# Kernel optimization log

Measured on AMD Instinct MI355X. Metric: run time of the kernel, lower is better.

Reference implementation:

```python
import jax, jax.numpy as jnp
import numpy as np

# ---- static config (must match init_kwargs) ----
DIM = 256
DIM_K = 16
N = 32          # window size: hh = ww = N
HEADS = 8
DIM_OUT = 256
DIM_U = 1
DIM_V = DIM_OUT // HEADS  # 32
EPS = 1e-5
N2 = N * N


def _calc_rel_pos(n):
    # pos: (n*n, 2) of (i, j) coords, rel: (n*n, n*n, 2) shifted by n-1
    pos = np.stack(np.meshgrid(np.arange(n), np.arange(n), indexing='ij'), axis=-1).reshape(-1, 2)
    rel = pos[None, :, :] - pos[:, None, :] + (n - 1)
    return rel.astype(np.int32)

_REL = _calc_rel_pos(N)  # (N2, N2, 2)


def _cplx(re, im):
    return jax.lax.complex(re, im)


def _complex_bn(x, scale, shift):
    # x: (b, c, m) complex. Complex batchnorm: var = E[x^2] - E[x]^2 (complex square).
    mean = x.mean(axis=(0, 2))                       # (c,)
    var = (x ** 2).mean(axis=(0, 2)) - mean ** 2     # (c,) complex
    xn = (x - mean[None, :, None]) / jnp.sqrt(var + EPS)[None, :, None]
    return scale[None, :, None] * xn + shift[None, :, None]


def setup_inputs() -> dict:
    key = jax.random.key(0)
    ks = jax.random.split(key, 18)
    f = jnp.float32
    b = 16
    mk = lambda k, shape, s=1.0: (jax.random.normal(k, shape, dtype=f) * s)
    inp = {
        'x_re': mk(ks[0], (b, DIM, N, N)),
        'x_im': mk(ks[1], (b, DIM, N, N)),
        # 1x1 conv weights, stored as (out_ch, in_ch)
        'wq_re': mk(ks[2], (DIM_K * HEADS, DIM), DIM ** -0.5),
        'wq_im': mk(ks[3], (DIM_K * HEADS, DIM), DIM ** -0.5),
        'wk_re': mk(ks[4], (DIM_K * DIM_U, DIM), DIM ** -0.5),
        'wk_im': mk(ks[5], (DIM_K * DIM_U, DIM), DIM ** -0.5),
        'wv_re': mk(ks[6], (DIM_V * DIM_U, DIM), DIM ** -0.5),
        'wv_im': mk(ks[7], (DIM_V * DIM_U, DIM), DIM ** -0.5),
        # complex BN affine params (init: scale=1+0j, shift=0)
        'qs_re': jnp.ones((DIM_K * HEADS,), f),
        'qs_im': jnp.zeros((DIM_K * HEADS,), f),
        'qb_re': jnp.zeros((DIM_K * HEADS,), f),
        'qb_im': jnp.zeros((DIM_K * HEADS,), f),
        'vs_re': jnp.ones((DIM_V * DIM_U,), f),
        'vs_im': jnp.zeros((DIM_V * DIM_U,), f),
        'vb_re': jnp.zeros((DIM_V * DIM_U,), f),
        'vb_im': jnp.zeros((DIM_V * DIM_U,), f),
        # rel-pos embedding table (2n-1, 2n-1, k, u)
        'emb_re': mk(ks[8], (2 * N - 1, 2 * N - 1, DIM_K, DIM_U)),
        'emb_im': mk(ks[9], (2 * N - 1, 2 * N - 1, DIM_K, DIM_U)),
    }
    return inp


def reference(x_re, x_im, wq_re, wq_im, wk_re, wk_im, wv_re, wv_im,
              qs_re, qs_im, qb_re, qb_im, vs_re, vs_im, vb_re, vb_im,
              emb_re, emb_im):
    x = _cplx(x_re, x_im)                       # (b, c, N, N)
    b = x.shape[0]
    xf = x.reshape(b, DIM, N2)                  # (b, c, m)

    wq = _cplx(wq_re, wq_im)
    wk = _cplx(wk_re, wk_im)
    wv = _cplx(wv_re, wv_im)

    q = jnp.einsum('oc,bcm->bom', wq, xf)       # (b, k*h, m)
    k = jnp.einsum('oc,bcm->bom', wk, xf)       # (b, k*u, m)
    v = jnp.einsum('oc,bcm->bom', wv, xf)       # (b, v*u, m)

    q = _complex_bn(q, _cplx(qs_re, qs_im), _cplx(qb_re, qb_im))
    v = _complex_bn(v, _cplx(vs_re, vs_im), _cplx(vb_re, vb_im))

    q = q.reshape(b, HEADS, DIM_K, N2)          # b h k n
    k = k.reshape(b, DIM_U, DIM_K, N2)          # b u k m
    v = v.reshape(b, DIM_U, DIM_V, N2)          # b u v m

    k = jax.nn.softmax(jnp.abs(k), axis=-1).astype(jnp.complex64)

    lam_c = jnp.einsum('bukm,buvm->bkv', k, v)          # content lambda
    Yc = jnp.einsum('bhkn,bkv->bhvn', q, lam_c)

    emb = _cplx(emb_re, emb_im)
    remb = emb[_REL[..., 0], _REL[..., 1]]              # (n, m, k, u) gathered
    lam_p = jnp.einsum('nmku,buvm->bnkv', remb, v)      # positional lambdas
    Yp = jnp.einsum('bhkn,bnkv->bhvn', q, lam_p)

    Y = Yc + Yp                                          # (b, h, v, n)
    out = Y.reshape(b, HEADS * DIM_V, N, N)             # b (h v) hh ww
    return out
```

## Files before the change

### kernel.cpp

```cpp
#include <hip/hip_runtime.h>
#include <math.h>

#define DIMC 256
#define NCH  176
#define MM   1024
#define BB   16
#define KD   16
#define HH   8
#define VD   32
#define EPSV 1e-5
#define OPAD 192

typedef short short8 __attribute__((ext_vector_type(8)));
typedef float f32x4  __attribute__((ext_vector_type(4)));
typedef unsigned u32x4v __attribute__((ext_vector_type(4)));

union frag8 { unsigned u[4]; short8 s; u32x4v v; };

__device__ __forceinline__ unsigned bf16rne(float f) {
    unsigned u = __float_as_uint(f);
    unsigned r = u + 0x7FFFu + ((u >> 16) & 1u);
    return r >> 16;
}
__device__ __forceinline__ float bf16tof(unsigned h) {
    return __uint_as_float(h << 16);
}

#define GL2LDS16(g, l) __builtin_amdgcn_global_load_lds( \
    (const __attribute__((address_space(1))) unsigned*)(g), \
    (__attribute__((address_space(3))) unsigned*)(l), 16, 0, 0)
#define GL2LDS4(g, l) __builtin_amdgcn_global_load_lds( \
    (const __attribute__((address_space(1))) unsigned*)(g), \
    (__attribute__((address_space(3))) unsigned*)(l), 4, 0, 0)

__global__ __launch_bounds__(256) void k_wprep(
    const float* __restrict__ wq_re, const float* __restrict__ wq_im,
    const float* __restrict__ wk_re, const float* __restrict__ wk_im,
    const float* __restrict__ wv_re, const float* __restrict__ wv_im,
    unsigned* __restrict__ Wpk)
{
    int idx = blockIdx.x * 256 + threadIdx.x;
    if (idx >= OPAD * 128) return;
    int o = idx >> 7, j = idx & 127;
    int c0 = 2 * j;
    float r0 = 0.f, r1 = 0.f, i0 = 0.f, i1 = 0.f;
    if (o < 128) {
        r0 = wq_re[o * DIMC + c0]; r1 = wq_re[o * DIMC + c0 + 1];
        i0 = wq_im[o * DIMC + c0]; i1 = wq_im[o * DIMC + c0 + 1];
    } else if (o < 144) {
        int oo = o - 128;
        r0 = wk_re[oo * DIMC + c0]; r1 = wk_re[oo * DIMC + c0 + 1];
        i0 = wk_im[oo * DIMC + c0]; i1 = wk_im[oo * DIMC + c0 + 1];
    } else if (o < 176) {
        int oo = o - 144;
        r0 = wv_re[oo * DIMC + c0]; r1 = wv_re[oo * DIMC + c0 + 1];
        i0 = wv_im[oo * DIMC + c0]; i1 = wv_im[oo * DIMC + c0 + 1];
    }
    unsigned rh0 = bf16rne(r0), rh1 = bf16rne(r1);
    unsigned ih0 = bf16rne(i0), ih1 = bf16rne(i1);
    float rl0 = r0 - bf16tof(rh0), rl1 = r1 - bf16tof(rh1);
    float il0 = i0 - bf16tof(ih0), il1 = i1 - bf16tof(ih1);
    Wpk[0 * OPAD * 128 + idx] = rh0 | (rh1 << 16);
    Wpk[1 * OPAD * 128 + idx] = ih0 | (ih1 << 16);
    Wpk[2 * OPAD * 128 + idx] = bf16rne(rl0) | (bf16rne(rl1) << 16);
    Wpk[3 * OPAD * 128 + idx] = bf16rne(il0) | (bf16rne(il1) << 16);
}

__global__ __launch_bounds__(256, 2) void k_proj(
    const float* __restrict__ x_re, const float* __restrict__ x_im,
    const unsigned* __restrict__ Wpk,
    float2* __restrict__ O)
{
    const int m0  = blockIdx.x * 32;
    const int b   = blockIdx.y;
    const int tid = threadIdx.x;
    const int w    = tid >> 6;
    const int lane = tid & 63;
    const int quad = lane >> 4;
    const int col  = lane & 15;
    const int mt = w & 1, og = w >> 1;

    __shared__ __align__(16) unsigned Wsh[4 * OPAD * 16];
    __shared__ __align__(16) unsigned Xsh[4 * 32 * 20];

    f32x4 accR[6], accI[6];
#pragma unroll
    for (int t = 0; t < 6; ++t) {
        accR[t] = (f32x4){0.f, 0.f, 0.f, 0.f};
        accI[t] = (f32x4){0.f, 0.f, 0.f, 0.f};
    }

    const int ms = tid & 31;
    const int cps = tid >> 5;

#pragma unroll 1
    for (int kk = 0; kk < 8; ++kk) {
#pragma unroll
        for (int p = 0; p < 12; ++p) {
            int idx = p * 256 + tid;
            int plane = idx / 768;
            int rem = idx - plane * 768;
            int row = rem >> 2, seg = rem & 3;
            u32x4v d = *(const u32x4v*)&Wpk[(size_t)plane * (OPAD * 128) + row * 128 + kk * 16 + seg * 4];
            *(u32x4v*)&Wsh[(plane * OPAD + row) * 16 + seg * 4] = d;
        }
#pragma unroll
        for (int p = 0; p < 2; ++p) {
            int cp = cps + p * 8;
            int c  = kk * 32 + cp * 2;
            size_t base = ((size_t)(b * DIMC + c)) * MM + m0 + ms;
            float r0 = x_re[base],      i0 = x_im[base];
            float r1 = x_re[base + MM], i1 = x_im[base + MM];
            unsigned rh0 = bf16rne(r0), rh1 = bf16rne(r1);
            unsigned ih0 = bf16rne(i0), ih1 = bf16rne(i1);
            float rl0 = r0 - bf16tof(rh0), rl1 = r1 - bf16tof(rh1);
            float il0 = i0 - bf16tof(ih0), il1 = i1 - bf16tof(ih1);
            Xsh[0 * 640 + ms * 20 + cp] = rh0 | (rh1 << 16);
            Xsh[1 * 640 + ms * 20 + cp] = ih0 | (ih1 << 16);
            Xsh[2 * 640 + ms * 20 + cp] = bf16rne(rl0) | (bf16rne(rl1) << 16);
            Xsh[3 * 640 + ms * 20 + cp] = bf16rne(il0) | (bf16rne(il1) << 16);
        }
        __syncthreads();

        int mrow = mt * 16 + col;
        short8 Xrh = *(const short8*)&Xsh[0 * 640 + mrow * 20 + quad * 4];
        short8 Xih = *(const short8*)&Xsh[1 * 640 + mrow * 20 + quad * 4];
        short8 Xrl = *(const short8*)&Xsh[2 * 640 + mrow * 20 + quad * 4];
        short8 Xil = *(const short8*)&Xsh[3 * 640 + mrow * 20 + quad * 4];

#pragma unroll
        for (int ot = 0; ot < 6; ++ot) {
            int orow = (og * 6 + ot) * 16 + col;
            frag8 Arh, Aih, Arl, Ail, Anh, Anl;
            Arh.s = *(const short8*)&Wsh[(0 * OPAD + orow) * 16 + quad * 4];
            Aih.s = *(const short8*)&Wsh[(1 * OPAD + orow) * 16 + quad * 4];
            Arl.s = *(const short8*)&Wsh[(2 * OPAD + orow) * 16 + quad * 4];
            Ail.s = *(const short8*)&Wsh[(3 * OPAD + orow) * 16 + quad * 4];
#pragma unroll
            for (int i = 0; i < 4; ++i) {
                Anh.u[i] = Aih.u[i] ^ 0x80008000u;
                Anl.u[i] = Ail.u[i] ^ 0x80008000u;
            }
            accR[ot] = __builtin_amdgcn_mfma_f32_16x16x32_bf16(Arh.s, Xrh, accR[ot], 0, 0, 0);
            accR[ot] = __builtin_amdgcn_mfma_f32_16x16x32_bf16(Anh.s, Xih, accR[ot], 0, 0, 0);
            accR[ot] = __builtin_amdgcn_mfma_f32_16x16x32_bf16(Arh.s, Xrl, accR[ot], 0, 0, 0);
            accR[ot] = __builtin_amdgcn_mfma_f32_16x16x32_bf16(Anh.s, Xil, accR[ot], 0, 0, 0);
            accR[ot] = __builtin_amdgcn_mfma_f32_16x16x32_bf16(Arl.s, Xrh, accR[ot], 0, 0, 0);
            accR[ot] = __builtin_amdgcn_mfma_f32_16x16x32_bf16(Anl.s, Xih, accR[ot], 0, 0, 0);
            accI[ot] = __builtin_amdgcn_mfma_f32_16x16x32_bf16(Arh.s, Xih, accI[ot], 0, 0, 0);
            accI[ot] = __builtin_amdgcn_mfma_f32_16x16x32_bf16(Aih.s, Xrh, accI[ot], 0, 0, 0);
            accI[ot] = __builtin_amdgcn_mfma_f32_16x16x32_bf16(Arh.s, Xil, accI[ot], 0, 0, 0);
            accI[ot] = __builtin_amdgcn_mfma_f32_16x16x32_bf16(Aih.s, Xrl, accI[ot], 0, 0, 0);
            accI[ot] = __builtin_amdgcn_mfma_f32_16x16x32_bf16(Arl.s, Xih, accI[ot], 0, 0, 0);
            accI[ot] = __builtin_amdgcn_mfma_f32_16x16x32_bf16(Ail.s, Xrh, accI[ot], 0, 0, 0);
        }
        __syncthreads();
    }

#pragma unroll
    for (int ot = 0; ot < 6; ++ot) {
        int gto = og * 6 + ot;
        if (gto >= 11) continue;
#pragma unroll
        for (int r = 0; r < 4; ++r) {
            int o = gto * 16 + quad * 4 + r;
            O[((size_t)(b * NCH + o)) * MM + m0 + mt * 16 + col] =
                make_float2(accR[ot][r], accI[ot][r]);
        }
    }
}

__global__ __launch_bounds__(256) void k_bnstats(
    const float2* __restrict__ O,
    const float* __restrict__ qs_re, const float* __restrict__ qs_im,
    const float* __restrict__ qb_re, const float* __restrict__ qb_im,
    const float* __restrict__ vs_re, const float* __restrict__ vs_im,
    const float* __restrict__ vb_re, const float* __restrict__ vb_im,
    float4* __restrict__ stats)
{
    const int ch  = blockIdx.x;
    const int o   = (ch < 128) ? ch : (144 + ch - 128);
    const int tid = threadIdx.x;

    double sr = 0, si = 0, sq = 0, sri = 0;
    for (int idx = tid; idx < BB * MM; idx += 256) {
        int b = idx >> 10, m = idx & 1023;
        float2 val = O[((size_t)(b * NCH + o)) * MM + m];
        double r = val.x, ii = val.y;
        sr += r; si += ii; sq += r * r - ii * ii; sri += r * ii;
    }
    __shared__ double red[4][256];
    red[0][tid] = sr; red[1][tid] = si; red[2][tid] = sq; red[3][tid] = sri;
    __syncthreads();
    for (int s = 128; s > 0; s >>= 1) {
        if (tid < s) {
            red[0][tid] += red[0][tid + s]; red[1][tid] += red[1][tid + s];
            red[2][tid] += red[2][tid + s]; red[3][tid] += red[3][tid + s];
        }
        __syncthreads();
    }
    if (tid == 0) {
        const double inv = 1.0 / (double)(BB * MM);
        double mr = red[0][0] * inv, mi = red[1][0] * inv;
        double vr = red[2][0] * inv - (mr * mr - mi * mi) + EPSV;
        double vi = 2.0 * (red[3][0] * inv - mr * mi);
        double rad = sqrt(vr * vr + vi * vi);
        double wr  = sqrt(fmax(0.5 * (rad + vr), 0.0));
        double wi  = sqrt(fmax(0.5 * (rad - vr), 0.0));
        if (vi < 0) wi = -wi;
        double den = wr * wr + wi * wi;
        double ivr = wr / den, ivi = -wi / den;
        double scr, sci, shr, shi;
        if (ch < 128) { scr = qs_re[ch]; sci = qs_im[ch]; shr = qb_re[ch]; shi = qb_im[ch]; }
        else { int i2 = ch - 128; scr = vs_re[i2]; sci = vs_im[i2]; shr = vb_re[i2]; shi = vb_im[i2]; }
        double Ar = scr * ivr - sci * ivi;
        double Ai = scr * ivi + sci * ivr;
        double Br = shr - (Ar * mr - Ai * mi);
        double Bi = shi - (Ar * mi + Ai * mr);
        stats[ch] = make_float4((float)Ar, (float)Ai, (float)Br, (float)Bi);
    }
}

__global__ __launch_bounds__(256) void k_bnapply(
    const float4* __restrict__ stats, float2* __restrict__ O,
    unsigned* __restrict__ VR, unsigned* __restrict__ VI)
{
    int ch = blockIdx.x, b = blockIdx.y;
    int o  = (ch < 128) ? ch : (144 + ch - 128);
    float4 s = stats[ch];
    float2* row = O + ((size_t)(b * NCH + o)) * MM;
    int tid = threadIdx.x;
    for (int mm = tid; mm < 512; mm += 256) {
        float4 two = *(float4*)&row[2 * mm];
        float nr0 = s.x * two.x - s.y * two.y + s.z;
        float ni0 = s.x * two.y + s.y * two.x + s.w;
        float nr1 = s.x * two.z - s.y * two.w + s.z;
        float ni1 = s.x * two.w + s.y * two.z + s.w;
        *(float4*)&row[2 * mm] = make_float4(nr0, ni0, nr1, ni1);
        if (ch >= 128) {
            int bv = b * VD + (ch - 128);
            int cC = mm >> 4, off = mm & 15;
            int u = off >> 2, oo = off & 3;
            int sl = (((u ^ (bv & 3)) << 2) | oo);
            size_t idx = ((size_t)cC * 512 + bv) * 16 + sl;
            VR[idx] = bf16rne(nr0) | (bf16rne(nr1) << 16);
            VI[idx] = bf16rne(ni0) | (bf16rne(ni1) << 16);
        }
    }
}

__global__ __launch_bounds__(256) void k_softlam(
    const float2* __restrict__ O, float2* __restrict__ lamc)
{
    int kc = blockIdx.x, b = blockIdx.y;
    const float2* row = O + ((size_t)(b * NCH + 128 + kc)) * MM;
    int tid = threadIdx.x;
    __shared__ float red[256];
    __shared__ float skl[1024];

    float mag[4]; float mx = -1e30f;
#pragma unroll
    for (int j = 0; j < 4; ++j) {
        float2 v = row[tid + j * 256];
        mag[j] = sqrtf(v.x * v.x + v.y * v.y);
        mx = fmaxf(mx, mag[j]);
    }
    red[tid] = mx; __syncthreads();
    for (int s = 128; s > 0; s >>= 1) { if (tid < s) red[tid] = fmaxf(red[tid], red[tid + s]); __syncthreads(); }
    mx = red[0]; __syncthreads();
    float e[4]; float sum = 0.f;
#pragma unroll
    for (int j = 0; j < 4; ++j) { e[j] = expf(mag[j] - mx); sum += e[j]; }
    red[tid] = sum; __syncthreads();
    for (int s = 128; s > 0; s >>= 1) { if (tid < s) red[tid] += red[tid + s]; __syncthreads(); }
    float inv = 1.f / red[0];
#pragma unroll
    for (int j = 0; j < 4; ++j) skl[tid + j * 256] = e[j] * inv;
    __syncthreads();

    int v = tid >> 3, s8 = tid & 7;
    const float2* vrow = O + ((size_t)(b * NCH + 144 + v)) * MM;
    float ar = 0.f, ai = 0.f;
    for (int i = 0; i < 128; ++i) {
        int m = s8 * 128 + i;
        float wgt = skl[m]; float2 vv = vrow[m];
        ar += wgt * vv.x; ai += wgt * vv.y;
    }
    __shared__ float2 part[32][8];
    part[v][s8] = make_float2(ar, ai);
    __syncthreads();
    if (tid < 32) {
        float2 t = part[tid][0];
#pragma unroll
        for (int j = 1; j < 8; ++j) { t.x += part[tid][j].x; t.y += part[tid][j].y; }
        lamc[((size_t)(b * KD + kc)) * VD + tid] = t;
    }
}

__global__ __launch_bounds__(256) void k_eprepD(
    const float* __restrict__ er, const float* __restrict__ ei,
    unsigned* __restrict__ embD)
{
    int idx = blockIdx.x * 256 + threadIdx.x;
    if (idx >= 8 * 63 * 768) return;
    int s   = idx % 48;
    int k   = (idx / 48) % 16;
    int di  = (idx / 768) % 63;
    int win = idx / (768 * 63);
    int u_s = s >> 2, o = s & 3;
    int p   = (((k >> 1) & 1) << 1) | ((k >> 2) & 1);
    int dj2 = ((u_s ^ p) << 2) | o;
    int dj  = 28 - win * 4 + dj2;
    unsigned val = 0;
    if (dj <= 62) {
        int e = (di * 63 + dj) * 16 + k;
        val = bf16rne(er[e]) | (bf16rne(ei[e]) << 16);
    }
    embD[idx] = val;
}

__global__ __launch_bounds__(256, 2) void k_main(
    const float2* __restrict__ O,
    const unsigned* __restrict__ embD,
    const unsigned* __restrict__ VbfR,
    const unsigned* __restrict__ VbfI,
    const float2* __restrict__ lamc,
    float* __restrict__ out, int cplx)
{
    const int tid  = threadIdx.x;
    const int w    = tid >> 6;
    const int lane = tid & 63;
    const int quad = lane >> 4;
    const int col  = lane & 15;

    const int n0  = blockIdx.x * 4;
    const int bvq = blockIdx.y;
    const int b0  = bvq * 4;
    const int ni  = n0 >> 5;
    const int nj0 = n0 & 31;
    const int win = nj0 >> 2;

    __shared__ __align__(16) unsigned shraw[2 * 4864];
    __shared__ __align__(16) float2 qsh[2048];

#pragma unroll
    for (int it = 0; it < 8; ++it) {
        int idx = it * 256 + tid;
        int g = idx & 3, ch = (idx >> 2) & 127, bl = idx >> 9;
        qsh[idx] = O[((size_t)((b0 + bl) * NCH + ch)) * MM + n0 + g];
    }

    f32x4 accr[4][2], acci[4][2];
#pragma unroll
    for (int g = 0; g < 4; ++g)
#pragma unroll
        for (int t = 0; t < 2; ++t) {
            accr[g][t] = (f32x4){0.f, 0.f, 0.f, 0.f};
            acci[g][t] = (f32x4){0.f, 0.f, 0.f, 0.f};
        }

    const unsigned* vR0 = VbfR + (size_t)bvq * 2048 + w * 512 + lane * 4;
    const unsigned* vI0 = VbfI + (size_t)bvq * 2048 + w * 512 + lane * 4;
    const unsigned* eD0 = embD + (size_t)win * (63 * 768) + w * 64 + lane;

    const int p     = (((col >> 1) & 1) << 1) | ((col >> 2) & 1);
    const int aBase = col * 48;
    const int a0 = aBase + (((2 * quad)     ^ p) << 2);
    const int a1 = aBase + (((2 * quad + 1) ^ p) << 2);
    const int a2 = aBase + (((2 * quad + 2) ^ p) << 2);
    const int bswz  = (quad ^ (col & 3)) << 2;
    const int rowb0 = (w * 32 + col) * 16 + bswz;
    const int rowb1 = (w * 32 + 16 + col) * 16 + bswz;

    {
        unsigned* vr = shraw;
        unsigned* vi = shraw + 2048;
        unsigned* es = shraw + 4096;
        GL2LDS16(vR0,       vr + w * 512);
        GL2LDS16(vR0 + 256, vr + w * 512 + 256);
        GL2LDS16(vI0,       vi + w * 512);
        GL2LDS16(vI0 + 256, vi + w * 512 + 256);
        const unsigned* gE = eD0 + (size_t)(31 - ni) * 768;
        GL2LDS4(gE,       es + w * 64);
        GL2LDS4(gE + 256, es + 256 + w * 64);
        GL2LDS4(gE + 512, es + 512 + w * 64);
    }

#pragma unroll 1
    for (int c = 0; c < 32; ++c) {
        __syncthreads();

        if (c + 1 < 32) {
            unsigned* vr = shraw + ((c + 1) & 1) * 4864;
            unsigned* vi = vr + 2048;
            unsigned* es = vr + 4096;
            const unsigned* gR = vR0 + (size_t)(c + 1) * 8192;
            const unsigned* gI = vI0 + (size_t)(c + 1) * 8192;
            GL2LDS16(gR,       vr + w * 512);
            GL2LDS16(gR + 256, vr + w * 512 + 256);
            GL2LDS16(gI,       vi + w * 512);
            GL2LDS16(gI + 256, vi + w * 512 + 256);
            const unsigned* gE = eD0 + (size_t)(c + 1 - ni + 31) * 768;
            GL2LDS4(gE,       es + w * 64);
            GL2LDS4(gE + 256, es + 256 + w * 64);
            GL2LDS4(gE + 512, es + 512 + w * 64);
        }

        const unsigned* vr = shraw + (c & 1) * 4864;
        const unsigned* vi = vr + 2048;
        const unsigned* es = vr + 4096;

        short8 Br0 = *(const short8*)&vr[rowb0];
        short8 Br1 = *(const short8*)&vr[rowb1];
        short8 Bi0 = *(const short8*)&vi[rowb0];
        short8 Bi1 = *(const short8*)&vi[rowb1];

        u32x4v W0 = *(const u32x4v*)&es[a0];
        u32x4v W1 = *(const u32x4v*)&es[a1];
        u32x4v W2 = *(const u32x4v*)&es[a2];
        unsigned W[12] = { W0.x, W0.y, W0.z, W0.w,
                           W1.x, W1.y, W1.z, W1.w,
                           W2.x, W2.y, W2.z, W2.w };

#pragma unroll
        for (int g = 0; g < 4; ++g) {
            const int o = 3 - g;
            union { unsigned u[4]; short8 s; } Rr, Ri, Rin;
            Rr.u[0] = __builtin_amdgcn_perm(W[o + 1], W[o + 0], 0x05040100u);
            Rr.u[1] = __builtin_amdgcn_perm(W[o + 3], W[o + 2], 0x05040100u);
            Rr.u[2] = __builtin_amdgcn_perm(W[o + 5], W[o + 4], 0x05040100u);
            Rr.u[3] = __builtin_amdgcn_perm(W[o + 7], W[o + 6], 0x05040100u);
            Ri.u[0] = __builtin_amdgcn_perm(W[o + 1], W[o + 0], 0x07060302u);
            Ri.u[1] = __builtin_amdgcn_perm(W[o + 3], W[o + 2], 0x07060302u);
            Ri.u[2] = __builtin_amdgcn_perm(W[o + 5], W[o + 4], 0x07060302u);
            Ri.u[3] = __builtin_amdgcn_perm(W[o + 7], W[o + 6], 0x07060302u);
            Rin.u[0] = Ri.u[0] ^ 0x80008000u;
            Rin.u[1] = Ri.u[1] ^ 0x80008000u;
            Rin.u[2] = Ri.u[2] ^ 0x80008000u;
            Rin.u[3] = Ri.u[3] ^ 0x80008000u;
            accr[g][0] = __builtin_amdgcn_mfma_f32_16x16x32_bf16(Rr.s,  Br0, accr[g][0], 0, 0, 0);
            accr[g][0] = __builtin_amdgcn_mfma_f32_16x16x32_bf16(Rin.s, Bi0, accr[g][0], 0, 0, 0);
            acci[g][0] = __builtin_amdgcn_mfma_f32_16x16x32_bf16(Rr.s,  Bi0, acci[g][0], 0, 0, 0);
            acci[g][0] = __builtin_amdgcn_mfma_f32_16x16x32_bf16(Ri.s,  Br0, acci[g][0], 0, 0, 0);
            accr[g][1] = __builtin_amdgcn_mfma_f32_16x16x32_bf16(Rr.s,  Br1, accr[g][1], 0, 0, 0);
            accr[g][1] = __builtin_amdgcn_mfma_f32_16x16x32_bf16(Rin.s, Bi1, accr[g][1], 0, 0, 0);
            acci[g][1] = __builtin_amdgcn_mfma_f32_16x16x32_bf16(Rr.s,  Bi1, acci[g][1], 0, 0, 0);
            acci[g][1] = __builtin_amdgcn_mfma_f32_16x16x32_bf16(Ri.s,  Br1, acci[g][1], 0, 0, 0);
        }
    }

    float2 lcv[2][4];
#pragma unroll
    for (int t = 0; t < 2; ++t) {
        int bvl = w * 32 + t * 16 + col;
        int bloc = b0 + (bvl >> 5), v = bvl & 31;
#pragma unroll
        for (int r = 0; r < 4; ++r)
            lcv[t][r] = lamc[((size_t)(bloc * KD + quad * 4 + r)) * VD + v];
    }

    float2* lamt = (float2*)shraw;
    const int col128 = tid & 127;
    const int hb = (tid >> 7) * 4;
    const int bl = col128 >> 5, vY = col128 & 31;
    const int bY = b0 + bl;
    float2* op2 = (float2*)out;
#pragma unroll
    for (int g = 0; g < 4; ++g) {
        __syncthreads();
#pragma unroll
        for (int t = 0; t < 2; ++t) {
            int bvl = w * 32 + t * 16 + col;
#pragma unroll
            for (int r = 0; r < 4; ++r) {
                int k = quad * 4 + r;
                lamt[k * 128 + bvl] = make_float2(accr[g][t][r] + lcv[t][r].x,
                                                  acci[g][t][r] + lcv[t][r].y);
            }
        }
        __syncthreads();
        float yr[4], yi[4];
#pragma unroll
        for (int h = 0; h < 4; ++h) { yr[h] = 0.f; yi[h] = 0.f; }
#pragma unroll
        for (int k = 0; k < 16; ++k) {
            float2 l = lamt[k * 128 + col128];
#pragma unroll
            for (int h = 0; h < 4; ++h) {
                float2 q = qsh[(bl * 128 + (hb + h) * 16 + k) * 4 + g];
                yr[h] += q.x * l.x - q.y * l.y;
                yi[h] += q.x * l.y + q.y * l.x;
            }
        }
        int n = n0 + g;
        if (cplx) {
#pragma unroll
            for (int h = 0; h < 4; ++h)
                op2[((size_t)(bY * 256 + (hb + h) * 32 + vY)) * MM + n] = make_float2(yr[h], yi[h]);
        } else {
#pragma unroll
            for (int h = 0; h < 4; ++h)
                out[((size_t)(bY * 256 + (hb + h) * 32 + vY)) * MM + n] = yr[h];
        }
    }
}

extern "C" void kernel_launch(void* const* d_in, const int* in_sizes, int n_in,
                              void* d_out, int out_size, void* d_ws, size_t ws_size,
                              hipStream_t stream)
{
    const float* x_re  = (const float*)d_in[0];
    const float* x_im  = (const float*)d_in[1];
    const float* wq_re = (const float*)d_in[2];
    const float* wq_im = (const float*)d_in[3];
    const float* wk_re = (const float*)d_in[4];
    const float* wk_im = (const float*)d_in[5];
    const float* wv_re = (const float*)d_in[6];
    const float* wv_im = (const float*)d_in[7];
    const float* qs_re = (const float*)d_in[8];
    const float* qs_im = (const float*)d_in[9];
    const float* qb_re = (const float*)d_in[10];
    const float* qb_im = (const float*)d_in[11];
    const float* vs_re = (const float*)d_in[12];
    const float* vs_im = (const float*)d_in[13];
    const float* vb_re = (const float*)d_in[14];
    const float* vb_im = (const float*)d_in[15];
    const float* emb_re = (const float*)d_in[16];
    const float* emb_im = (const float*)d_in[17];

    float* ws = (float*)d_ws;
    const size_t O_OFF  = 0;
    const size_t ST_OFF = O_OFF + (size_t)BB * NCH * MM * 2;
    const size_t LC_OFF = ST_OFF + 640;
    const size_t WP_OFF = LC_OFF + 16384;
    const size_t VR_OFF = WP_OFF + 98304;
    const size_t VI_OFF = VR_OFF + 262144;
    const size_t ED_OFF = VI_OFF + 262144;

    float2*   O     = (float2*)(ws + O_OFF);
    float4*   stats = (float4*)(ws + ST_OFF);
    float2*   lamc  = (float2*)(ws + LC_OFF);
    unsigned* Wpk   = (unsigned*)(ws + WP_OFF);
    unsigned* VbfR  = (unsigned*)(ws + VR_OFF);
    unsigned* VbfI  = (unsigned*)(ws + VI_OFF);
    unsigned* embD  = (unsigned*)(ws + ED_OFF);
    float*    outp  = (float*)d_out;

    int cplx = (out_size >= 2 * BB * 256 * MM) ? 1 : 0;

    k_wprep<<<dim3(96), 256, 0, stream>>>(wq_re, wq_im, wk_re, wk_im,
                                          wv_re, wv_im, Wpk);
    k_eprepD<<<dim3(1512), 256, 0, stream>>>(emb_re, emb_im, embD);
    k_proj<<<dim3(32, BB), 256, 0, stream>>>(x_re, x_im, Wpk, O);
    k_bnstats<<<dim3(160), 256, 0, stream>>>(O, qs_re, qs_im, qb_re, qb_im,
                                             vs_re, vs_im, vb_re, vb_im, stats);
    k_bnapply<<<dim3(160, BB), 256, 0, stream>>>(stats, O, VbfR, VbfI);
    k_softlam<<<dim3(KD, BB), 256, 0, stream>>>(O, lamc);
    k_main<<<dim3(256, 4), 256, 0, stream>>>(O, embD, VbfR, VbfI, lamc, outp, cplx);
}
```

Before: 282.9 us.

## Load V fragments directly to registers, vectorize X loads, shrink LDS footprint

```diff
diff --git a/kernel.cpp b/kernel.cpp
--- a/kernel.cpp
+++ b/kernel.cpp
@@ -29,9 +29,6 @@
 #define GL2LDS16(g, l) __builtin_amdgcn_global_load_lds( \
     (const __attribute__((address_space(1))) unsigned*)(g), \
     (__attribute__((address_space(3))) unsigned*)(l), 16, 0, 0)
-#define GL2LDS4(g, l) __builtin_amdgcn_global_load_lds( \
-    (const __attribute__((address_space(1))) unsigned*)(g), \
-    (__attribute__((address_space(3))) unsigned*)(l), 4, 0, 0)
 
 __global__ __launch_bounds__(256) void k_wprep(
     const float* __restrict__ wq_re, const float* __restrict__ wq_im,
@@ -90,8 +87,9 @@
         accI[t] = (f32x4){0.f, 0.f, 0.f, 0.f};
     }
 
-    const int ms = tid & 31;
-    const int cps = tid >> 5;
+    const int cl = tid >> 3;
+    const int m4 = (tid & 7) * 4;
+    const int cp = cl >> 1, half = cl & 1;
 
 #pragma unroll 1
     for (int kk = 0; kk < 8; ++kk) {
@@ -104,21 +102,24 @@
             u32x4v d = *(const u32x4v*)&Wpk[(size_t)plane * (OPAD * 128) + row * 128 + kk * 16 + seg * 4];
             *(u32x4v*)&Wsh[(plane * OPAD + row) * 16 + seg * 4] = d;
         }
-#pragma unroll
-        for (int p = 0; p < 2; ++p) {
-            int cp = cps + p * 8;
-            int c  = kk * 32 + cp * 2;
-            size_t base = ((size_t)(b * DIMC + c)) * MM + m0 + ms;
-            float r0 = x_re[base],      i0 = x_im[base];
-            float r1 = x_re[base + MM], i1 = x_im[base + MM];
-            unsigned rh0 = bf16rne(r0), rh1 = bf16rne(r1);
-            unsigned ih0 = bf16rne(i0), ih1 = bf16rne(i1);
-            float rl0 = r0 - bf16tof(rh0), rl1 = r1 - bf16tof(rh1);
-            float il0 = i0 - bf16tof(ih0), il1 = i1 - bf16tof(ih1);
-            Xsh[0 * 640 + ms * 20 + cp] = rh0 | (rh1 << 16);
-            Xsh[1 * 640 + ms * 20 + cp] = ih0 | (ih1 << 16);
-            Xsh[2 * 640 + ms * 20 + cp] = bf16rne(rl0) | (bf16rne(rl1) << 16);
-            Xsh[3 * 640 + ms * 20 + cp] = bf16rne(il0) | (bf16rne(il1) << 16);
+        {
+            size_t base = ((size_t)(b * DIMC + kk * 32 + cl)) * MM + m0 + m4;
+            float4 xr = *(const float4*)&x_re[base];
+            float4 xi = *(const float4*)&x_im[base];
+            unsigned short* xs = (unsigned short*)Xsh;
+            const float* xrf = (const float*)&xr;
+            const float* xif = (const float*)&xi;
+#pragma unroll
+            for (int j = 0; j < 4; ++j) {
+                float r = xrf[j], iv = xif[j];
+                unsigned rh = bf16rne(r), ih = bf16rne(iv);
+                float rl = r - bf16tof(rh), il = iv - bf16tof(ih);
+                int m = m4 + j;
+                xs[(0 * 640 + m * 20 + cp) * 2 + half] = (unsigned short)rh;
+                xs[(1 * 640 + m * 20 + cp) * 2 + half] = (unsigned short)ih;
+                xs[(2 * 640 + m * 20 + cp) * 2 + half] = (unsigned short)bf16rne(rl);
+                xs[(3 * 640 + m * 20 + cp) * 2 + half] = (unsigned short)bf16rne(il);
+            }
         }
         __syncthreads();
 
@@ -240,9 +241,7 @@
         if (ch >= 128) {
             int bv = b * VD + (ch - 128);
             int cC = mm >> 4, off = mm & 15;
-            int u = off >> 2, oo = off & 3;
-            int sl = (((u ^ (bv & 3)) << 2) | oo);
-            size_t idx = ((size_t)cC * 512 + bv) * 16 + sl;
+            size_t idx = ((size_t)cC * 512 + bv) * 16 + off;
             VR[idx] = bf16rne(nr0) | (bf16rne(nr1) << 16);
             VI[idx] = bf16rne(ni0) | (bf16rne(ni1) << 16);
         }
@@ -340,15 +339,8 @@
     const int nj0 = n0 & 31;
     const int win = nj0 >> 2;
 
-    __shared__ __align__(16) unsigned shraw[2 * 4864];
-    __shared__ __align__(16) float2 qsh[2048];
-
-#pragma unroll
-    for (int it = 0; it < 8; ++it) {
-        int idx = it * 256 + tid;
-        int g = idx & 3, ch = (idx >> 2) & 127, bl = idx >> 9;
-        qsh[idx] = O[((size_t)((b0 + bl) * NCH + ch)) * MM + n0 + g];
-    }
+    __shared__ __align__(16) unsigned embS[2][768];
+    __shared__ __align__(16) float2 lamqs[4096];
 
     f32x4 accr[4][2], acci[4][2];
 #pragma unroll
@@ -359,62 +351,45 @@
             acci[g][t] = (f32x4){0.f, 0.f, 0.f, 0.f};
         }
 
-    const unsigned* vR0 = VbfR + (size_t)bvq * 2048 + w * 512 + lane * 4;
-    const unsigned* vI0 = VbfI + (size_t)bvq * 2048 + w * 512 + lane * 4;
-    const unsigned* eD0 = embD + (size_t)win * (63 * 768) + w * 64 + lane;
-
-    const int p     = (((col >> 1) & 1) << 1) | ((col >> 2) & 1);
+    const unsigned* vR = VbfR + ((size_t)(bvq * 128 + w * 32 + col)) * 16 + quad * 4;
+    const unsigned* vI = VbfI + ((size_t)(bvq * 128 + w * 32 + col)) * 16 + quad * 4;
+
+    const unsigned* eDw = embD + (size_t)win * (63 * 768);
+
+    const int p  = (((col >> 1) & 1) << 1) | ((col >> 2) & 1);
     const int aBase = col * 48;
     const int a0 = aBase + (((2 * quad)     ^ p) << 2);
     const int a1 = aBase + (((2 * quad + 1) ^ p) << 2);
     const int a2 = aBase + (((2 * quad + 2) ^ p) << 2);
-    const int bswz  = (quad ^ (col & 3)) << 2;
-    const int rowb0 = (w * 32 + col) * 16 + bswz;
-    const int rowb1 = (w * 32 + 16 + col) * 16 + bswz;
-
-    {
-        unsigned* vr = shraw;
-        unsigned* vi = shraw + 2048;
-        unsigned* es = shraw + 4096;
-        GL2LDS16(vR0,       vr + w * 512);
-        GL2LDS16(vR0 + 256, vr + w * 512 + 256);
-        GL2LDS16(vI0,       vi + w * 512);
-        GL2LDS16(vI0 + 256, vi + w * 512 + 256);
-        const unsigned* gE = eD0 + (size_t)(31 - ni) * 768;
-        GL2LDS4(gE,       es + w * 64);
-        GL2LDS4(gE + 256, es + 256 + w * 64);
-        GL2LDS4(gE + 512, es + 512 + w * 64);
-    }
+
+    if (w < 3)
+        GL2LDS16(eDw + (size_t)(31 - ni) * 768 + w * 256 + lane * 4,
+                 (unsigned*)embS[0] + w * 256);
+    frag8 cBr0, cBr1, cBi0, cBi1;
+    cBr0.v = *(const u32x4v*)(vR);
+    cBr1.v = *(const u32x4v*)(vR + 256);
+    cBi0.v = *(const u32x4v*)(vI);
+    cBi1.v = *(const u32x4v*)(vI + 256);
 
 #pragma unroll 1
     for (int c = 0; c < 32; ++c) {
         __syncthreads();
 
-        if (c + 1 < 32) {
-            unsigned* vr = shraw + ((c + 1) & 1) * 4864;
-            unsigned* vi = vr + 2048;
-            unsigned* es = vr + 4096;
-            const unsigned* gR = vR0 + (size_t)(c + 1) * 8192;
-            const unsigned* gI = vI0 + (size_t)(c + 1) * 8192;
-            GL2LDS16(gR,       vr + w * 512);
-            GL2LDS16(gR + 256, vr + w * 512 + 256);
-            GL2LDS16(gI,       vi + w * 512);
-            GL2LDS16(gI + 256, vi + w * 512 + 256);
-            const unsigned* gE = eD0 + (size_t)(c + 1 - ni + 31) * 768;
-            GL2LDS4(gE,       es + w * 64);
-            GL2LDS4(gE + 256, es + 256 + w * 64);
-            GL2LDS4(gE + 512, es + 512 + w * 64);
-        }
-
-        const unsigned* vr = shraw + (c & 1) * 4864;
-        const unsigned* vi = vr + 2048;
-        const unsigned* es = vr + 4096;
-
-        short8 Br0 = *(const short8*)&vr[rowb0];
-        short8 Br1 = *(const short8*)&vr[rowb1];
-        short8 Bi0 = *(const short8*)&vi[rowb0];
-        short8 Bi1 = *(const short8*)&vi[rowb1];
-
+        const int cn = (c + 1 < 32) ? (c + 1) : 31;
+        if (w < 3)
+            GL2LDS16(eDw + (size_t)(cn - ni + 31) * 768 + w * 256 + lane * 4,
+                     (unsigned*)embS[cn & 1] + w * 256);
+        frag8 nBr0, nBr1, nBi0, nBi1;
+        {
+            const unsigned* r  = vR + (size_t)cn * 8192;
+            const unsigned* ii = vI + (size_t)cn * 8192;
+            nBr0.v = *(const u32x4v*)(r);
+            nBr1.v = *(const u32x4v*)(r + 256);
+            nBi0.v = *(const u32x4v*)(ii);
+            nBi1.v = *(const u32x4v*)(ii + 256);
+        }
+
+        const unsigned* es = (const unsigned*)embS[c & 1];
         u32x4v W0 = *(const u32x4v*)&es[a0];
         u32x4v W1 = *(const u32x4v*)&es[a1];
         u32x4v W2 = *(const u32x4v*)&es[a2];
@@ -438,15 +413,23 @@
             Rin.u[1] = Ri.u[1] ^ 0x80008000u;
             Rin.u[2] = Ri.u[2] ^ 0x80008000u;
             Rin.u[3] = Ri.u[3] ^ 0x80008000u;
-            accr[g][0] = __builtin_amdgcn_mfma_f32_16x16x32_bf16(Rr.s,  Br0, accr[g][0], 0, 0, 0);
-            accr[g][0] = __builtin_amdgcn_mfma_f32_16x16x32_bf16(Rin.s, Bi0, accr[g][0], 0, 0, 0);
-            acci[g][0] = __builtin_amdgcn_mfma_f32_16x16x32_bf16(Rr.s,  Bi0, acci[g][0], 0, 0, 0);
-            acci[g][0] = __builtin_amdgcn_mfma_f32_16x16x32_bf16(Ri.s,  Br0, acci[g][0], 0, 0, 0);
-            accr[g][1] = __builtin_amdgcn_mfma_f32_16x16x32_bf16(Rr.s,  Br1, accr[g][1], 0, 0, 0);
-            accr[g][1] = __builtin_amdgcn_mfma_f32_16x16x32_bf16(Rin.s, Bi1, accr[g][1], 0, 0, 0);
-            acci[g][1] = __builtin_amdgcn_mfma_f32_16x16x32_bf16(Rr.s,  Bi1, acci[g][1], 0, 0, 0);
-            acci[g][1] = __builtin_amdgcn_mfma_f32_16x16x32_bf16(Ri.s,  Br1, acci[g][1], 0, 0, 0);
-        }
+            accr[g][0] = __builtin_amdgcn_mfma_f32_16x16x32_bf16(Rr.s,  cBr0.s, accr[g][0], 0, 0, 0);
+            accr[g][0] = __builtin_amdgcn_mfma_f32_16x16x32_bf16(Rin.s, cBi0.s, accr[g][0], 0, 0, 0);
+            acci[g][0] = __builtin_amdgcn_mfma_f32_16x16x32_bf16(Rr.s,  cBi0.s, acci[g][0], 0, 0, 0);
+            acci[g][0] = __builtin_amdgcn_mfma_f32_16x16x32_bf16(Ri.s,  cBr0.s, acci[g][0], 0, 0, 0);
+            accr[g][1] = __builtin_amdgcn_mfma_f32_16x16x32_bf16(Rr.s,  cBr1.s, accr[g][1], 0, 0, 0);
+            accr[g][1] = __builtin_amdgcn_mfma_f32_16x16x32_bf16(Rin.s, cBi1.s, accr[g][1], 0, 0, 0);
+            acci[g][1] = __builtin_amdgcn_mfma_f32_16x16x32_bf16(Rr.s,  cBi1.s, acci[g][1], 0, 0, 0);
+            acci[g][1] = __builtin_amdgcn_mfma_f32_16x16x32_bf16(Ri.s,  cBr1.s, acci[g][1], 0, 0, 0);
+        }
+        cBr0 = nBr0; cBr1 = nBr1; cBi0 = nBi0; cBi1 = nBi1;
+    }
+
+#pragma unroll
+    for (int it = 0; it < 8; ++it) {
+        int idx = it * 256 + tid;
+        int g = idx & 3, ch = (idx >> 2) & 127, bl = idx >> 9;
+        lamqs[2048 + idx] = O[((size_t)((b0 + bl) * NCH + ch)) * MM + n0 + g];
     }
 
     float2 lcv[2][4];
@@ -459,7 +442,8 @@
             lcv[t][r] = lamc[((size_t)(bloc * KD + quad * 4 + r)) * VD + v];
     }
 
-    float2* lamt = (float2*)shraw;
+    float2* lamt = lamqs;
+    float2* qsh  = lamqs + 2048;
     const int col128 = tid & 127;
     const int hb = (tid >> 7) * 4;
     const int bl = col128 >> 5, vY = col128 & 31;
```

New measurement: 284.6 us. Within noise of the previous version (+0.6%).
